# Performance work log

Measured on AMD Instinct MI355X. Metric: run time of the kernel, lower is better.

## Reference

```python
import jax, jax.numpy as jnp
import numpy as np
import math

B, S, HID, NH = 2, 2048, 1024, 16
HD = HID // NH


def setup_inputs() -> dict:
    key = jax.random.key(0)
    ks = jax.random.split(key, 6)
    scale = 0.02
    return {
        "hidden_states": jax.random.normal(ks[0], (B, S, HID), dtype=jnp.float32),
        "attention_mask": jnp.ones((B, S), dtype=jnp.float32),
        "Wq": jax.random.normal(ks[1], (HID, HID), dtype=jnp.float32) * scale,
        "bq": jnp.zeros((HID,), dtype=jnp.float32),
        "Wk": jax.random.normal(ks[2], (HID, HID), dtype=jnp.float32) * scale,
        "bk": jnp.zeros((HID,), dtype=jnp.float32),
        "Wv": jax.random.normal(ks[3], (HID, HID), dtype=jnp.float32) * scale,
        "bv": jnp.zeros((HID,), dtype=jnp.float32),
        "Wo": jax.random.normal(ks[4], (HID, HID), dtype=jnp.float32) * scale,
        "bo": jnp.zeros((HID,), dtype=jnp.float32),
        "beta": jnp.zeros((1,), dtype=jnp.float32),
        "gamma": jnp.ones((1,), dtype=jnp.float32),
    }


def reference(hidden_states, attention_mask, Wq, bq, Wk, bk, Wv, bv, Wo, bo, beta, gamma):
    b, s, h = hidden_states.shape

    def proj(W, bias):
        # torch Linear: x @ W.T + b ; then split heads -> [B, NH, S, HD]
        y = jnp.einsum('bsh,oh->bso', hidden_states, W) + bias
        return y.reshape(b, s, NH, HD).transpose(0, 2, 1, 3)

    q = proj(Wq, bq)
    k = proj(Wk, bk)
    v = proj(Wv, bv)

    scores = jnp.einsum('bnsd,bntd->bnst', q, k) / math.sqrt(HD)  # [B,NH,S,S]
    # extended mask: [B,1,1,S]; additive -1e4 on masked positions
    scores = scores + (1.0 - attention_mask)[:, None, None, :] * (-10000.0)

    # ConsMax: exp(scores - beta - rowmax) / gamma (no sum normalization)
    shifted = scores - beta
    shifted = shifted - jnp.max(shifted, axis=-1, keepdims=True)
    probs = jnp.exp(shifted) / gamma  # dropout p=0 -> identity

    ctx = jnp.einsum('bnst,bntd->bnsd', probs, v)  # [B,NH,S,HD]
    ctx = ctx.transpose(0, 2, 1, 3).reshape(b, s, h)
    return jnp.einsum('bsh,oh->bso', ctx, Wo) + bo
```

## Files before the change

kernel.cpp:

```cpp
#include <hip/hip_runtime.h>
#include <hip/hip_bf16.h>


typedef unsigned short u16;
typedef __attribute__((ext_vector_type(8))) short short8;
typedef __attribute__((ext_vector_type(4))) float floatx4;
typedef __attribute__((ext_vector_type(16))) float floatx16;
typedef __attribute__((ext_vector_type(2))) unsigned uintx2;

constexpr int B_  = 2;
constexpr int S_  = 2048;
constexpr int HID = 1024;
constexpr int NH  = 16;
constexpr int HD  = 64;

constexpr float LOG2E   = 1.4426950408889634f;
constexpr float QSCALE  = 0.125f * LOG2E;
constexpr float MSCALE  = -10000.0f * LOG2E;

#if __has_builtin(__builtin_amdgcn_exp2f)
#define EXP2(x) __builtin_amdgcn_exp2f(x)
#else
#define EXP2(x) exp2f(x)
#endif

__device__ __forceinline__ u16 f2us(float f) {
    union { float f; unsigned int i; } x;
    x.f = f;
    unsigned int r = x.i + 0x7FFFu + ((x.i >> 16) & 1u);
    return (u16)(r >> 16);
}
__device__ __forceinline__ unsigned pk2(float a, float b) {
    __hip_bfloat162 h = __float22bfloat162_rn(make_float2(a, b));
    unsigned u; __builtin_memcpy(&u, &h, 4); return u;
}
#if __has_builtin(__builtin_amdgcn_permlane32_swap)
__device__ __forceinline__ uintx2 pswap2(unsigned a, unsigned c) {
    return __builtin_amdgcn_permlane32_swap(a, c, false, false);
}
#else
__device__ __forceinline__ uintx2 pswap2(unsigned a, unsigned c) {
    asm volatile("v_permlane32_swap_b32 %0, %1\n\ts_nop 1" : "+v"(a), "+v"(c));
    return (uintx2){a, c};
}
#endif
__device__ __forceinline__ void async_lds16(const u16* g, u16* l) {
    __builtin_amdgcn_global_load_lds(
        (const __attribute__((address_space(1))) unsigned int*)g,
        (__attribute__((address_space(3))) unsigned int*)l, 16, 0, 0);
}

__global__ __launch_bounds__(256)
void cvt_all(const float* __restrict__ hs, const float* __restrict__ Wq,
             const float* __restrict__ Wk, const float* __restrict__ Wv,
             const float* __restrict__ Wo,
             u16* __restrict__ hs_bf, u16* __restrict__ Wcat,
             u16* __restrict__ Wo_bf)
{
    const int bid = blockIdx.x;
    const float* src;
    u16* dst;
    size_t base;
    if (bid < 4096) {
        src = hs; dst = hs_bf; base = (size_t)bid * 1024;
    } else if (bid < 7168) {
        const int s = (bid - 4096) >> 10;
        src = (s == 0) ? Wq : (s == 1) ? Wk : Wv;
        dst = Wcat + (size_t)s * 1048576;
        base = (size_t)((bid - 4096) & 1023) * 1024;
    } else {
        src = Wo; dst = Wo_bf; base = (size_t)(bid - 7168) * 1024;
    }
    const size_t i = base + threadIdx.x * 4;
    float4 t = *(const float4*)(src + i);
    uint2 o = { pk2(t.x, t.y), pk2(t.z, t.w) };
    *(uint2*)(dst + i) = o;
}

__global__ __launch_bounds__(256)
void qkv_gemm(const u16* __restrict__ hs_bf, const u16* __restrict__ Wcat,
              const float* __restrict__ bq, const float* __restrict__ bk,
              const float* __restrict__ bv,
              u16* __restrict__ Qo, u16* __restrict__ Ko, u16* __restrict__ VT)
{
    __shared__ u16 Alds[3][4096];
    __shared__ u16 Blds[3][4096];

    const int tid = threadIdx.x;
    const int id  = blockIdx.x;
    const int xcd = id & 7, jb = id >> 3;
    const int m0  = (xcd * 4 + (jb & 3)) * 128;
    const int n0g = (jb >> 2) * 128;
    const int p   = n0g >> 10;
    const int n0  = n0g & 1023;
    const u16*   Wb = Wcat + (size_t)p * 1048576;
    const float* bi = (p == 0) ? bq : (p == 1) ? bk : bv;
    const float  osc = (p == 0) ? QSCALE : 1.0f;

    const int w = tid >> 6, l = tid & 63;
    const int quad = l >> 4, l16 = l & 15;
    const int wy = w >> 1, wx = w & 1;

    floatx4 acc[4][4];
    #pragma unroll
    for (int i = 0; i < 4; ++i)
        #pragma unroll
        for (int j = 0; j < 4; ++j) acc[i][j] = (floatx4){0.f, 0.f, 0.f, 0.f};

    auto stage = [&](int ks, int bf) {
        const int k0 = ks * 32;
        #pragma unroll
        for (int c = 0; c < 2; ++c) {
            const int s = w * 2 + c;
            async_lds16(hs_bf + (size_t)(m0 + s * 16 + l16) * HID + k0 + quad * 8,
                        &Alds[bf][s * 512]);
            async_lds16(Wb + (size_t)(n0 + s * 16 + l16) * HID + k0 + quad * 8,
                        &Blds[bf][s * 512]);
        }
    };

    constexpr int NS = HID / 32;
    stage(0, 0);
    stage(1, 1);

    for (int ks = 0; ks < NS; ++ks) {
        const int cur = ks % 3;
        if (ks < NS - 1) asm volatile("s_waitcnt vmcnt(4)" ::: "memory");
        else             asm volatile("s_waitcnt vmcnt(0)" ::: "memory");
        __builtin_amdgcn_s_barrier();
        if (ks + 2 < NS) stage(ks + 2, (ks + 2) % 3);

        short8 afr[4], bfr[4];
        #pragma unroll
        for (int i = 0; i < 4; ++i)
            afr[i] = *(const short8*)&Alds[cur][(wy * 4 + i) * 512 + l * 8];
        #pragma unroll
        for (int j = 0; j < 4; ++j)
            bfr[j] = *(const short8*)&Blds[cur][(wx * 4 + j) * 512 + l * 8];
        #pragma unroll
        for (int i = 0; i < 4; ++i)
            #pragma unroll
            for (int j = 0; j < 4; ++j)
                acc[i][j] = __builtin_amdgcn_mfma_f32_16x16x32_bf16(afr[i], bfr[j], acc[i][j], 0, 0, 0);
    }

    #pragma unroll
    for (int i = 0; i < 4; ++i)
        #pragma unroll
        for (int j = 0; j < 4; ++j) {
            const int nn   = n0 + wx * 64 + j * 16 + l16;
            const int head = nn >> 6, dd = nn & 63;
            const float bb_ = bi[nn];
            const int mmb = m0 + wy * 64 + i * 16 + quad * 4;
            const int b = mmb >> 11, ss = mmb & (S_ - 1);
            if (p == 2) {
                uint2 st = { pk2(acc[i][j][0] + bb_, acc[i][j][1] + bb_),
                             pk2(acc[i][j][2] + bb_, acc[i][j][3] + bb_) };
                *(uint2*)(VT + (((size_t)(b * NH + head)) * HD + dd) * S_ + ss) = st;
            } else {
                u16* Out = (p == 0) ? Qo : Ko;
                #pragma unroll
                for (int rg = 0; rg < 4; ++rg)
                    Out[(((size_t)b * NH + head) * S_ + ss + rg) * HD + dd] =
                        f2us((acc[i][j][rg] + bb_) * osc);
            }
        }
}

__global__ __launch_bounds__(512, 4)
void attn16(const u16* __restrict__ Qg, const u16* __restrict__ Kg,
            const u16* __restrict__ VTg, const float* __restrict__ mask,
            const float* __restrict__ gamma, u16* __restrict__ ctx)
{
    __shared__ u16 SMEM[28672];
    u16*   KbB = SMEM;
    u16*   VbB = SMEM + 12288;
    float* Mb  = (float*)(SMEM + 24576);

    const int tid = threadIdx.x;
    const int w = tid >> 6, l = tid & 63;
    const int wq = w & 3, wk = w >> 2;
    const int l32 = l & 31, hh = l >> 5;
    const int id  = blockIdx.x;
    const int xcd = id & 7, jb = id >> 3;
    const int bh  = xcd * 4 + (jb >> 4);
    const int qb  = jb & 15;
    const int b0  = bh >> 4, h = bh & (NH - 1);

    const u16* Qb    = Qg  + (size_t)bh * S_ * HD;
    const u16* Kbg   = Kg  + (size_t)bh * S_ * HD;
    const u16* Vbg   = VTg + (size_t)bh * HD * S_;
    const float* mG  = mask + (size_t)b0 * S_;

    const int qrow = qb * 128 + wq * 32 + l32;

    short8 qB[4];
    #pragma unroll
    for (int dc = 0; dc < 4; ++dc)
        qB[dc] = *(const short8*)(Qb + (size_t)qrow * HD + dc * 16 + hh * 8);

    {
        float4 mv = *(const float4*)(mG + tid * 4);
        float* d = &Mb[tid * 4];
        d[0] = fmaf(mv.x, -MSCALE, MSCALE);
        d[1] = fmaf(mv.y, -MSCALE, MSCALE);
        d[2] = fmaf(mv.z, -MSCALE, MSCALE);
        d[3] = fmaf(mv.w, -MSCALE, MSCALE);
    }

    floatx16 oacc[2];
    #pragma unroll
    for (int db = 0; db < 2; ++db)
        #pragma unroll
        for (int i = 0; i < 16; ++i) oacc[db][i] = 0.f;
    float m_run = -1e30f;

    u16* Kbuf = KbB + wk * 6144;
    u16* Vbuf = VbB + wk * 6144;

    auto stage = [&](int i, int bf) {
        const int kt = 2 * i + wk;
        async_lds16(Kbg + (size_t)(kt * 32 + l32) * HD + wq * 16 + hh * 8,
                    Kbuf + bf * 2048 + wq * 512);
        const int db = wq >> 1, kg = wq & 1;
        async_lds16(Vbg + (size_t)(db * 32 + l32) * S_ + kt * 32 + kg * 16 + hh * 8,
                    Vbuf + bf * 2048 + wq * 512);
    };

    __syncthreads();
    constexpr int NI = 32;
    stage(0, 0);
    stage(1, 1);

    for (int i = 0; i < NI; ++i) {
        const int cur = i % 3;
        if (i < NI - 1) asm volatile("s_waitcnt vmcnt(2)" ::: "memory");
        else            asm volatile("s_waitcnt vmcnt(0)" ::: "memory");
        __builtin_amdgcn_s_barrier();
        if (i + 2 < NI) stage(i + 2, (i + 2) % 3);

        const int kt = 2 * i + wk;

        const float* mrow = &Mb[kt * 32 + 4 * hh];
        floatx16 acc;
        #pragma unroll
        for (int g = 0; g < 4; ++g) {
            float4 mv = *(const float4*)(mrow + g * 8);
            acc[4*g]   = mv.x;
            acc[4*g+1] = mv.y;
            acc[4*g+2] = mv.z;
            acc[4*g+3] = mv.w;
        }
        #pragma unroll
        for (int dc = 0; dc < 4; ++dc) {
            short8 kf = *(const short8*)&Kbuf[cur * 2048 + dc * 512 + l * 8];
            acc = __builtin_amdgcn_mfma_f32_32x32x16_bf16(kf, qB[dc], acc, 0, 0, 0);
        }

        float mr = m_run;
        #pragma unroll
        for (int ii = 0; ii < 16; ++ii) mr = fmaxf(mr, acc[ii]);
        m_run = mr;

        uintx2 s0 = pswap2(pk2(EXP2(acc[0]),  EXP2(acc[1])),
                           pk2(EXP2(acc[4]),  EXP2(acc[5])));
        uintx2 s1 = pswap2(pk2(EXP2(acc[2]),  EXP2(acc[3])),
                           pk2(EXP2(acc[6]),  EXP2(acc[7])));
        uintx2 s2 = pswap2(pk2(EXP2(acc[8]),  EXP2(acc[9])),
                           pk2(EXP2(acc[12]), EXP2(acc[13])));
        uintx2 s3 = pswap2(pk2(EXP2(acc[10]), EXP2(acc[11])),
                           pk2(EXP2(acc[14]), EXP2(acc[15])));
        union { unsigned u[4]; short8 s8; } pf0, pf1;
        pf0.u[0] = s0[0]; pf0.u[1] = s1[0]; pf0.u[2] = s0[1]; pf0.u[3] = s1[1];
        pf1.u[0] = s2[0]; pf1.u[1] = s3[0]; pf1.u[2] = s2[1]; pf1.u[3] = s3[1];

        #pragma unroll
        for (int db = 0; db < 2; ++db) {
            short8 vf0 = *(const short8*)&Vbuf[cur * 2048 + (db * 2 + 0) * 512 + l * 8];
            short8 vf1 = *(const short8*)&Vbuf[cur * 2048 + (db * 2 + 1) * 512 + l * 8];
            oacc[db] = __builtin_amdgcn_mfma_f32_32x32x16_bf16(vf0, pf0.s8, oacc[db], 0, 0, 0);
            oacc[db] = __builtin_amdgcn_mfma_f32_32x32x16_bf16(vf1, pf1.s8, oacc[db], 0, 0, 0);
        }
    }

    __syncthreads();
    float* OS = (float*)SMEM;
    if (wk == 1) {
        float* d = OS + (size_t)(wq * 64 + l) * 33;
        #pragma unroll
        for (int db = 0; db < 2; ++db)
            #pragma unroll
            for (int ii = 0; ii < 16; ++ii) d[db * 16 + ii] = oacc[db][ii];
        d[32] = m_run;
    }
    __syncthreads();
    if (wk == 0) {
        const float* s = OS + (size_t)(wq * 64 + l) * 33;
        #pragma unroll
        for (int db = 0; db < 2; ++db)
            #pragma unroll
            for (int ii = 0; ii < 16; ++ii) oacc[db][ii] += s[db * 16 + ii];
        m_run = fmaxf(m_run, s[32]);
        const float mx = fmaxf(m_run, __shfl_xor(m_run, 32, 64));
        const float si = EXP2(-mx) * (1.0f / gamma[0]);
        u16* crow = ctx + (size_t)(b0 * S_ + qrow) * HID + h * HD;
        #pragma unroll
        for (int db = 0; db < 2; ++db)
            #pragma unroll
            for (int g = 0; g < 4; ++g) {
                uint2 st = { pk2(oacc[db][g * 4 + 0] * si, oacc[db][g * 4 + 1] * si),
                             pk2(oacc[db][g * 4 + 2] * si, oacc[db][g * 4 + 3] * si) };
                *(uint2*)(crow + db * 32 + g * 8 + hh * 4) = st;
            }
    }
}

__global__ __launch_bounds__(256)
void out_gemm(const u16* __restrict__ ctx, const u16* __restrict__ Wo_bf,
              const float* __restrict__ bo, float* __restrict__ out)
{
    __shared__ u16 Alds[3][4096];
    __shared__ u16 Blds[3][2048];

    const int tid = threadIdx.x;
    const int id  = blockIdx.x;
    const int xcd = id & 7, jb = id >> 3;
    const int m0  = (xcd * 4 + (jb & 3)) * 128;
    const int n0  = (jb >> 2) * 64;

    const int w = tid >> 6, l = tid & 63;
    const int quad = l >> 4, l16 = l & 15;

    floatx4 acc[2][4];
    #pragma unroll
    for (int i = 0; i < 2; ++i)
        #pragma unroll
        for (int j = 0; j < 4; ++j) acc[i][j] = (floatx4){0.f, 0.f, 0.f, 0.f};

    auto stage = [&](int ks, int bf) {
        const int k0 = ks * 32;
        #pragma unroll
        for (int c = 0; c < 2; ++c) {
            const int s = w * 2 + c;
            async_lds16(ctx + (size_t)(m0 + s * 16 + l16) * HID + k0 + quad * 8,
                        &Alds[bf][s * 512]);
        }
        async_lds16(Wo_bf + (size_t)(n0 + w * 16 + l16) * HID + k0 + quad * 8,
                    &Blds[bf][w * 512]);
    };

    constexpr int NS = HID / 32;
    stage(0, 0);
    stage(1, 1);

    for (int ks = 0; ks < NS; ++ks) {
        const int cur = ks % 3;
        if (ks < NS - 1) asm volatile("s_waitcnt vmcnt(3)" ::: "memory");
        else             asm volatile("s_waitcnt vmcnt(0)" ::: "memory");
        __builtin_amdgcn_s_barrier();
        if (ks + 2 < NS) stage(ks + 2, (ks + 2) % 3);

        short8 afr[2], bfr[4];
        #pragma unroll
        for (int i = 0; i < 2; ++i)
            afr[i] = *(const short8*)&Alds[cur][(w * 2 + i) * 512 + l * 8];
        #pragma unroll
        for (int j = 0; j < 4; ++j)
            bfr[j] = *(const short8*)&Blds[cur][j * 512 + l * 8];
        #pragma unroll
        for (int i = 0; i < 2; ++i)
            #pragma unroll
            for (int j = 0; j < 4; ++j)
                acc[i][j] = __builtin_amdgcn_mfma_f32_16x16x32_bf16(afr[i], bfr[j], acc[i][j], 0, 0, 0);
    }

    #pragma unroll
    for (int i = 0; i < 2; ++i)
        #pragma unroll
        for (int j = 0; j < 4; ++j) {
            const int nn = n0 + j * 16 + l16;
            const float bb_ = bo[nn];
            #pragma unroll
            for (int rg = 0; rg < 4; ++rg) {
                const int mm = m0 + w * 32 + i * 16 + quad * 4 + rg;
                out[(size_t)mm * HID + nn] = acc[i][j][rg] + bb_;
            }
        }
}

extern "C" void kernel_launch(void* const* d_in, const int* in_sizes, int n_in,
                              void* d_out, int out_size, void* d_ws, size_t ws_size,
                              hipStream_t stream)
{
    const float* hs    = (const float*)d_in[0];
    const float* mask  = (const float*)d_in[1];
    const float* Wq    = (const float*)d_in[2];
    const float* bq    = (const float*)d_in[3];
    const float* Wk    = (const float*)d_in[4];
    const float* bk    = (const float*)d_in[5];
    const float* Wv    = (const float*)d_in[6];
    const float* bv    = (const float*)d_in[7];
    const float* Wo    = (const float*)d_in[8];
    const float* bo    = (const float*)d_in[9];
    const float* gamma = (const float*)d_in[11];
    float* out = (float*)d_out;

    const size_t tsz = (size_t)B_ * NH * S_ * HD;
    u16* q     = (u16*)d_ws;
    u16* vT    = q + tsz;
    u16* Wcat  = vT + tsz;
    u16* Wo_bf = Wcat + 3u * 1048576u;
    u16* ctx   = Wo_bf + 1048576u;
    u16* hs_bf = (u16*)d_out;
    u16* kbuf  = hs_bf + tsz;

    cvt_all<<<dim3(8192), 256, 0, stream>>>(hs, Wq, Wk, Wv, Wo, hs_bf, Wcat, Wo_bf);
    qkv_gemm<<<dim3(768), 256, 0, stream>>>(hs_bf, Wcat, bq, bk, bv, q, kbuf, vT);
    attn16<<<dim3(512), 512, 0, stream>>>(q, kbuf, vT, mask, gamma, ctx);
    out_gemm<<<dim3(512), 256, 0, stream>>>(ctx, Wo_bf, bo, out);
}
```

Measured before the change: 224.3 us.

## Use BK=64 double-buffered GEMM pipeline and 128x128 tiles for out projection

Both projection GEMMs now stage 64-wide K slices into two LDS buffers instead of 32-wide slices into three, which halves the number of barrier iterations but leaves only one stage of prefetch in flight. The output GEMM also grows its tile from 128x64 to 128x128 with a 2x2 wave layout, halving the grid to 256 blocks. The goal is more operand reuse per load and fewer synchronisations. The cost is less latency hiding and lower occupancy and parallelism for out_gemm.

```diff
diff --git a/kernel.cpp b/kernel.cpp
--- a/kernel.cpp
+++ b/kernel.cpp
@@ -83,8 +83,8 @@
               const float* __restrict__ bv,
               u16* __restrict__ Qo, u16* __restrict__ Ko, u16* __restrict__ VT)
 {
-    __shared__ u16 Alds[3][4096];
-    __shared__ u16 Blds[3][4096];
+    __shared__ u16 Alds[2][8192];
+    __shared__ u16 Blds[2][8192];
 
     const int tid = threadIdx.x;
     const int id  = blockIdx.x;
@@ -108,40 +108,44 @@
         for (int j = 0; j < 4; ++j) acc[i][j] = (floatx4){0.f, 0.f, 0.f, 0.f};
 
     auto stage = [&](int ks, int bf) {
-        const int k0 = ks * 32;
+        const int k0 = ks * 64;
         #pragma unroll
         for (int c = 0; c < 2; ++c) {
             const int s = w * 2 + c;
-            async_lds16(hs_bf + (size_t)(m0 + s * 16 + l16) * HID + k0 + quad * 8,
-                        &Alds[bf][s * 512]);
-            async_lds16(Wb + (size_t)(n0 + s * 16 + l16) * HID + k0 + quad * 8,
-                        &Blds[bf][s * 512]);
+            #pragma unroll
+            for (int t = 0; t < 2; ++t) {
+                async_lds16(hs_bf + (size_t)(m0 + s * 16 + l16) * HID + k0 + t * 32 + quad * 8,
+                            &Alds[bf][s * 1024 + t * 512]);
+                async_lds16(Wb + (size_t)(n0 + s * 16 + l16) * HID + k0 + t * 32 + quad * 8,
+                            &Blds[bf][s * 1024 + t * 512]);
+            }
         }
     };
 
-    constexpr int NS = HID / 32;
+    constexpr int NS = HID / 64;
     stage(0, 0);
-    stage(1, 1);
 
     for (int ks = 0; ks < NS; ++ks) {
-        const int cur = ks % 3;
-        if (ks < NS - 1) asm volatile("s_waitcnt vmcnt(4)" ::: "memory");
-        else             asm volatile("s_waitcnt vmcnt(0)" ::: "memory");
+        const int cur = ks & 1;
+        asm volatile("s_waitcnt vmcnt(0)" ::: "memory");
         __builtin_amdgcn_s_barrier();
-        if (ks + 2 < NS) stage(ks + 2, (ks + 2) % 3);
-
-        short8 afr[4], bfr[4];
-        #pragma unroll
-        for (int i = 0; i < 4; ++i)
-            afr[i] = *(const short8*)&Alds[cur][(wy * 4 + i) * 512 + l * 8];
-        #pragma unroll
-        for (int j = 0; j < 4; ++j)
-            bfr[j] = *(const short8*)&Blds[cur][(wx * 4 + j) * 512 + l * 8];
-        #pragma unroll
-        for (int i = 0; i < 4; ++i)
+        if (ks + 1 < NS) stage(ks + 1, cur ^ 1);
+
+        #pragma unroll
+        for (int t = 0; t < 2; ++t) {
+            short8 afr[4], bfr[4];
+            #pragma unroll
+            for (int i = 0; i < 4; ++i)
+                afr[i] = *(const short8*)&Alds[cur][(wy * 4 + i) * 1024 + t * 512 + l * 8];
             #pragma unroll
             for (int j = 0; j < 4; ++j)
-                acc[i][j] = __builtin_amdgcn_mfma_f32_16x16x32_bf16(afr[i], bfr[j], acc[i][j], 0, 0, 0);
+                bfr[j] = *(const short8*)&Blds[cur][(wx * 4 + j) * 1024 + t * 512 + l * 8];
+            #pragma unroll
+            for (int i = 0; i < 4; ++i)
+                #pragma unroll
+                for (int j = 0; j < 4; ++j)
+                    acc[i][j] = __builtin_amdgcn_mfma_f32_16x16x32_bf16(afr[i], bfr[j], acc[i][j], 0, 0, 0);
+        }
     }
 
     #pragma unroll
@@ -319,70 +323,75 @@
 void out_gemm(const u16* __restrict__ ctx, const u16* __restrict__ Wo_bf,
               const float* __restrict__ bo, float* __restrict__ out)
 {
-    __shared__ u16 Alds[3][4096];
-    __shared__ u16 Blds[3][2048];
+    __shared__ u16 Alds[2][8192];
+    __shared__ u16 Blds[2][8192];
 
     const int tid = threadIdx.x;
     const int id  = blockIdx.x;
     const int xcd = id & 7, jb = id >> 3;
     const int m0  = (xcd * 4 + (jb & 3)) * 128;
-    const int n0  = (jb >> 2) * 64;
+    const int n0  = (jb >> 2) * 128;
 
     const int w = tid >> 6, l = tid & 63;
     const int quad = l >> 4, l16 = l & 15;
-
-    floatx4 acc[2][4];
-    #pragma unroll
-    for (int i = 0; i < 2; ++i)
+    const int wy = w >> 1, wx = w & 1;
+
+    floatx4 acc[4][4];
+    #pragma unroll
+    for (int i = 0; i < 4; ++i)
         #pragma unroll
         for (int j = 0; j < 4; ++j) acc[i][j] = (floatx4){0.f, 0.f, 0.f, 0.f};
 
     auto stage = [&](int ks, int bf) {
-        const int k0 = ks * 32;
+        const int k0 = ks * 64;
         #pragma unroll
         for (int c = 0; c < 2; ++c) {
             const int s = w * 2 + c;
-            async_lds16(ctx + (size_t)(m0 + s * 16 + l16) * HID + k0 + quad * 8,
-                        &Alds[bf][s * 512]);
-        }
-        async_lds16(Wo_bf + (size_t)(n0 + w * 16 + l16) * HID + k0 + quad * 8,
-                    &Blds[bf][w * 512]);
+            #pragma unroll
+            for (int t = 0; t < 2; ++t) {
+                async_lds16(ctx + (size_t)(m0 + s * 16 + l16) * HID + k0 + t * 32 + quad * 8,
+                            &Alds[bf][s * 1024 + t * 512]);
+                async_lds16(Wo_bf + (size_t)(n0 + s * 16 + l16) * HID + k0 + t * 32 + quad * 8,
+                            &Blds[bf][s * 1024 + t * 512]);
+            }
+        }
     };
 
-    constexpr int NS = HID / 32;
+    constexpr int NS = HID / 64;
     stage(0, 0);
-    stage(1, 1);
 
     for (int ks = 0; ks < NS; ++ks) {
-        const int cur = ks % 3;
-        if (ks < NS - 1) asm volatile("s_waitcnt vmcnt(3)" ::: "memory");
-        else             asm volatile("s_waitcnt vmcnt(0)" ::: "memory");
+        const int cur = ks & 1;
+        asm volatile("s_waitcnt vmcnt(0)" ::: "memory");
         __builtin_amdgcn_s_barrier();
-        if (ks + 2 < NS) stage(ks + 2, (ks + 2) % 3);
-
-        short8 afr[2], bfr[4];
-        #pragma unroll
-        for (int i = 0; i < 2; ++i)
-            afr[i] = *(const short8*)&Alds[cur][(w * 2 + i) * 512 + l * 8];
-        #pragma unroll
-        for (int j = 0; j < 4; ++j)
-            bfr[j] = *(const short8*)&Blds[cur][j * 512 + l * 8];
-        #pragma unroll
-        for (int i = 0; i < 2; ++i)
+        if (ks + 1 < NS) stage(ks + 1, cur ^ 1);
+
+        #pragma unroll
+        for (int t = 0; t < 2; ++t) {
+            short8 afr[4], bfr[4];
+            #pragma unroll
+            for (int i = 0; i < 4; ++i)
+                afr[i] = *(const short8*)&Alds[cur][(wy * 4 + i) * 1024 + t * 512 + l * 8];
             #pragma unroll
             for (int j = 0; j < 4; ++j)
-                acc[i][j] = __builtin_amdgcn_mfma_f32_16x16x32_bf16(afr[i], bfr[j], acc[i][j], 0, 0, 0);
-    }
-
-    #pragma unroll
-    for (int i = 0; i < 2; ++i)
+                bfr[j] = *(const short8*)&Blds[cur][(wx * 4 + j) * 1024 + t * 512 + l * 8];
+            #pragma unroll
+            for (int i = 0; i < 4; ++i)
+                #pragma unroll
+                for (int j = 0; j < 4; ++j)
+                    acc[i][j] = __builtin_amdgcn_mfma_f32_16x16x32_bf16(afr[i], bfr[j], acc[i][j], 0, 0, 0);
+        }
+    }
+
+    #pragma unroll
+    for (int i = 0; i < 4; ++i)
         #pragma unroll
         for (int j = 0; j < 4; ++j) {
-            const int nn = n0 + j * 16 + l16;
+            const int nn = n0 + wx * 64 + j * 16 + l16;
             const float bb_ = bo[nn];
             #pragma unroll
             for (int rg = 0; rg < 4; ++rg) {
-                const int mm = m0 + w * 32 + i * 16 + quad * 4 + rg;
+                const int mm = m0 + wy * 64 + i * 16 + quad * 4 + rg;
                 out[(size_t)mm * HID + nn] = acc[i][j][rg] + bb_;
             }
         }
@@ -417,5 +426,5 @@
     cvt_all<<<dim3(8192), 256, 0, stream>>>(hs, Wq, Wk, Wv, Wo, hs_bf, Wcat, Wo_bf);
     qkv_gemm<<<dim3(768), 256, 0, stream>>>(hs_bf, Wcat, bq, bk, bv, q, kbuf, vT);
     attn16<<<dim3(512), 512, 0, stream>>>(q, kbuf, vT, mask, gamma, ctx);
-    out_gemm<<<dim3(512), 256, 0, stream>>>(ctx, Wo_bf, bo, out);
-}
+    out_gemm<<<dim3(256), 256, 0, stream>>>(ctx, Wo_bf, bo, out);
+}
```

Measured after the change: 248.2 us. +10.7%, slower.
